# Performance work log

Measured on AMD Instinct MI355X. Metric: run time of the kernel, lower is better.

The kernel has to match this reference:

```python
import jax, jax.numpy as jnp
import numpy as np

N_NODES = 50000
N_EDGES = 800000
N_GRAPHS = 512
IN_FEATS = 256
HIDDEN = 128
OUT_FEATS = 128


def _lin(key, fan_in, fan_out):
    return jax.random.normal(key, (fan_in, fan_out), jnp.float32) * (1.0 / np.sqrt(fan_in))


def setup_inputs() -> dict:
    key = jax.random.key(0)
    ks = jax.random.split(key, 16)
    x = jax.random.normal(ks[0], (N_NODES, IN_FEATS), jnp.float32)
    edge_index = jax.random.randint(ks[1], (2, N_EDGES), 0, N_NODES, jnp.int32)
    batch = jnp.sort(jax.random.randint(ks[2], (N_NODES,), 0, N_GRAPHS, jnp.int32))
    return {
        "x": x,
        "edge_index": edge_index,
        "batch": batch,
        "num_graphs": N_GRAPHS,
        # TD branch GCN params
        "td_W1": _lin(ks[3], IN_FEATS, HIDDEN), "td_b1": jnp.zeros((HIDDEN,), jnp.float32),
        "td_W2": _lin(ks[4], HIDDEN, OUT_FEATS), "td_b2": jnp.zeros((OUT_FEATS,), jnp.float32),
        # BU branch GCN params
        "bu_W1": _lin(ks[5], IN_FEATS, HIDDEN), "bu_b1": jnp.zeros((HIDDEN,), jnp.float32),
        "bu_W2": _lin(ks[6], HIDDEN, OUT_FEATS), "bu_b2": jnp.zeros((OUT_FEATS,), jnp.float32),
        # proj_head: Linear(256,256) -> ReLU -> Linear(256,128)
        "pw1": _lin(ks[7], OUT_FEATS * 2, 256), "pb1": jnp.zeros((256,), jnp.float32),
        "pw2": _lin(ks[8], 256, 128), "pb2": jnp.zeros((128,), jnp.float32),
    }


def gcn_conv(h_in, W, b, src, dst, n_nodes):
    """PyG GCNConv: self-loops + symmetric normalization D^-1/2 (A+I) D^-1/2 X W + b."""
    h = h_in @ W  # [N, out]
    ones = jnp.ones(src.shape[0], h.dtype)
    deg = jax.ops.segment_sum(ones, dst, num_segments=n_nodes) + 1.0  # +1 for self-loop
    dinv = jax.lax.rsqrt(deg)  # deg >= 1 always
    norm = dinv[src] * dinv[dst]  # [E]
    agg = jax.ops.segment_sum(h[src] * norm[:, None], dst, num_segments=n_nodes)
    agg = agg + h * (dinv * dinv)[:, None]  # self-loop edge contribution
    return agg + b


def reference(x, edge_index, batch, num_graphs,
              td_W1, td_b1, td_W2, td_b2,
              bu_W1, bu_b1, bu_W2, bu_b2,
              pw1, pb1, pw2, pb2):
    n = x.shape[0]
    src, dst = edge_index[0], edge_index[1]

    def branch(W1, b1, W2, b2, s, d):
        h = jax.nn.relu(gcn_conv(x, W1, b1, s, d, n))
        # dropout is identity in eval mode
        h = gcn_conv(h, W2, b2, s, d, n)
        return jax.ops.segment_sum(h, batch, num_segments=num_graphs)  # global_add_pool

    td = branch(td_W1, td_b1, td_W2, td_b2, src, dst)
    bu = branch(bu_W1, bu_b1, bu_W2, bu_b2, dst, src)  # flipped edge_index
    h = jnp.concatenate([bu, td], axis=1)  # [G, 2*out_feats]
    h = jax.nn.relu(h @ pw1 + pb1) @ pw2 + pb2
    return h
```

## Files before the change

kernel.cpp:

```cpp
#include <hip/hip_runtime.h>

#define N_NODES 50000
#define N_PAD   50048
#define N_EDGES 800000
#define N_GRAPHS 512
#define F_IN 256
#define F_H 128
#define F_CAT 256

#define BSHIFT 9
#define NB 98
#define CAP 10240
#define EPB 3125

#define NPAIR 16
#define SLICE_C 16
#define POOL_STRIDE ((size_t)N_PAD * SLICE_C)
#define AGG_CHUNK 128
#define N_GROUPS (N_NODES / 4)

typedef __attribute__((ext_vector_type(8))) short short8;
typedef __attribute__((ext_vector_type(4))) float f32x4;
typedef unsigned int uint;
typedef unsigned short ushort;

static __device__ __forceinline__ ushort f2bf(float f) {
    uint u = __float_as_uint(f);
    u += 0x7FFF + ((u >> 16) & 1);
    return (ushort)(u >> 16);
}
static __device__ __forceinline__ float bflo(uint v) { return __uint_as_float(v << 16); }
static __device__ __forceinline__ float bfhi(uint v) { return __uint_as_float(v & 0xFFFF0000u); }
static __device__ __forceinline__ float bfu(ushort v) { return __uint_as_float((uint)v << 16); }

#define GLL(g, l) __builtin_amdgcn_global_load_lds( \
    (const __attribute__((address_space(1))) unsigned int*)(g), \
    (__attribute__((address_space(3))) unsigned int*)(l), 16, 0, 0)

__global__ __launch_bounds__(256) void csr_scatter_kernel(
        const int* __restrict__ ei, int* __restrict__ gcur,
        uint* __restrict__ ebuf_td, uint* __restrict__ ebuf_bu) {
    __shared__ int lcnt[256];
    __shared__ int lbase[256];
    int tid = threadIdx.x;
    lcnt[tid] = 0;
    __syncthreads();
    int e0 = blockIdx.x * EPB;
    for (int k = tid; k < EPB; k += 256) {
        int i = e0 + k;
        int s = ei[i], d = ei[N_EDGES + i];
        atomicAdd(&lcnt[d >> BSHIFT], 1);
        atomicAdd(&lcnt[128 + (s >> BSHIFT)], 1);
    }
    __syncthreads();
    if (tid < 2 * NB) {
        int dir = tid / NB, b = tid % NB;
        int c = lcnt[dir * 128 + b];
        lbase[dir * 128 + b] = c ? atomicAdd(&gcur[dir * NB + b], c) : 0;
    }
    __syncthreads();
    lcnt[tid] = 0;
    __syncthreads();
    for (int k = tid; k < EPB; k += 256) {
        int i = e0 + k;
        int s = ei[i], d = ei[N_EDGES + i];
        int bd = d >> BSHIFT, bs = s >> BSHIFT;
        int p = atomicAdd(&lcnt[bd], 1) + lbase[bd];
        ebuf_td[(size_t)bd * CAP + p] = (uint)s | ((uint)(d & 511) << 16);
        int q = atomicAdd(&lcnt[128 + bs], 1) + lbase[128 + bs];
        ebuf_bu[(size_t)bs * CAP + q] = (uint)d | ((uint)(s & 511) << 16);
    }
}

__global__ __launch_bounds__(256) void csr_build_kernel(
        const uint* __restrict__ ebuf_td, const uint* __restrict__ ebuf_bu,
        const int* __restrict__ gcur,
        int* off_td, int* off_bu, ushort* deg_td, ushort* deg_bu,
        float* dinv_td, float* dinv_bu, ushort* csr_td, ushort* csr_bu) {
    int b = blockIdx.x, dir = blockIdx.y;
    const uint* ebuf = dir ? ebuf_bu : ebuf_td;
    int* off     = dir ? off_bu : off_td;
    ushort* deg  = dir ? deg_bu : deg_td;
    float* dinv  = dir ? dinv_bu : dinv_td;
    ushort* csr  = dir ? csr_bu : csr_td;
    __shared__ int cntL[512], offL[512], sm[256];
    int tid = threadIdx.x;
    cntL[tid] = 0; cntL[tid + 256] = 0;
    __syncthreads();
    int rbeg = b * CAP;
    int rend = rbeg + gcur[dir * NB + b];
    for (int k = rbeg + tid; k < rend; k += 256)
        atomicAdd(&cntL[ebuf[k] >> 16], 1);
    __syncthreads();
    int a0 = cntL[tid * 2], a1 = cntL[tid * 2 + 1];
    int ps = a0 + a1;
    sm[tid] = ps;
    __syncthreads();
    for (int o = 1; o < 256; o <<= 1) {
        int u = (tid >= o) ? sm[tid - o] : 0;
        __syncthreads();
        sm[tid] += u;
        __syncthreads();
    }
    int excl = sm[tid] - ps;
    offL[tid * 2] = excl;
    offL[tid * 2 + 1] = excl + a0;
    __syncthreads();
    int nbase = b << BSHIFT;
#pragma unroll
    for (int j = 0; j < 2; j++) {
        int nloc = tid + j * 256;
        int n = nbase + nloc;
        if (n < N_NODES) {
            off[n] = rbeg + offL[nloc];
            int c = cntL[nloc];
            deg[n] = (ushort)c;
            dinv[n] = rsqrtf((float)c + 1.0f);
        }
    }
    if (b == NB - 1) {
        int n = N_NODES + tid;
        if (n < N_PAD) dinv[n] = 1.0f;
    }
    cntL[tid] = offL[tid];
    cntL[tid + 256] = offL[tid + 256];
    __syncthreads();
    for (int k = rbeg + tid; k < rend; k += 256) {
        uint e = ebuf[k];
        int slot = atomicAdd(&cntL[e >> 16], 1);
        csr[rbeg + slot] = (ushort)(e & 0xFFFF);
    }
}

__global__ void prep_w_kernel(const float* __restrict__ td_W1, const float* __restrict__ bu_W1,
                              const float* __restrict__ td_W2, const float* __restrict__ bu_W2,
                              ushort* __restrict__ Bt1, ushort* __restrict__ Wt2) {
    int n = blockIdx.x;
    int k = threadIdx.x;
    float w1 = (n < F_H) ? td_W1[(size_t)k * F_H + n] : bu_W1[(size_t)k * F_H + (n - F_H)];
    Bt1[(size_t)n * 256 + k] = f2bf(w1);
    if (k < 128) {
        float w2 = (n < F_H) ? bu_W2[(size_t)k * F_H + n]
                             : td_W2[(size_t)k * F_H + (n - F_H)];
        Wt2[(size_t)k * 256 + n] = f2bf(w2);
    }
}

__global__ __launch_bounds__(256) void gemm_mfma(
        const float* __restrict__ x, const ushort* __restrict__ Bt,
        ushort* __restrict__ C,
        const float* __restrict__ dinv_td, const float* __restrict__ dinv_bu) {
    __shared__ __align__(16) ushort As[128 * 32];
    __shared__ __align__(16) ushort Bs[128 * 32];
    int tid = threadIdx.x;
    int wave = tid >> 6, lane = tid & 63, quad = lane >> 4, l16 = lane & 15;
    size_t bm = (size_t)blockIdx.x * 128;
    size_t bn = (size_t)blockIdx.y * 128;
    int br = blockIdx.y;
    const float* dsel = br ? dinv_bu : dinv_td;

    f32x4 acc[2][8];
    const f32x4 z4 = {0.f, 0.f, 0.f, 0.f};
#pragma unroll
    for (int i = 0; i < 2; i++)
#pragma unroll
        for (int j = 0; j < 8; j++) acc[i][j] = z4;

    int ar = tid >> 3;
    int akq = (tid & 7) * 4;
    int cb0 = wave * 64;
    int cb1 = 256 + wave * 64;
    int c0 = cb0 + lane, c1 = cb1 + lane;
    int r0 = c0 >> 2, s0 = (c0 & 3) * 8;
    int r1 = c1 >> 2, s1 = (c1 & 3) * 8;
    const ushort* b0p = Bt + (bn + r0) * 256 + s0;
    const ushort* b1p = Bt + (bn + r1) * 256 + s1;
    ushort* lB0 = Bs + cb0 * 8;
    ushort* lB1 = Bs + cb1 * 8;

    for (int kb = 0; kb < 8; kb++) {
        int k0 = kb * 32;
        float4 av[4];
#pragma unroll
        for (int j = 0; j < 4; j++) {
            size_t grow = bm + ar + j * 32;
            if (grow < N_NODES)
                av[j] = *(const float4*)(x + grow * F_IN + k0 + akq);
            else
                av[j] = make_float4(0.f, 0.f, 0.f, 0.f);
        }
        __syncthreads();
        GLL(b0p + k0, lB0);
        GLL(b1p + k0, lB1);
#pragma unroll
        for (int j = 0; j < 4; j++) {
            ushort4 u;
            u.x = f2bf(av[j].x); u.y = f2bf(av[j].y);
            u.z = f2bf(av[j].z); u.w = f2bf(av[j].w);
            *(ushort4*)(As + (ar + j * 32) * 32 + akq) = u;
        }
        __syncthreads();
        short8 af0 = *(const short8*)(As + (wave * 32 + l16) * 32 + quad * 8);
        short8 af1 = *(const short8*)(As + (wave * 32 + 16 + l16) * 32 + quad * 8);
#pragma unroll
        for (int ct = 0; ct < 8; ct++) {
            short8 bfr = *(const short8*)(Bs + (ct * 16 + l16) * 32 + quad * 8);
            acc[0][ct] = __builtin_amdgcn_mfma_f32_16x16x32_bf16(af0, bfr, acc[0][ct], 0, 0, 0);
            acc[1][ct] = __builtin_amdgcn_mfma_f32_16x16x32_bf16(af1, bfr, acc[1][ct], 0, 0, 0);
        }
    }
#pragma unroll
    for (int rt = 0; rt < 2; rt++) {
#pragma unroll
        for (int r = 0; r < 4; r++) {
            size_t row = bm + wave * 32 + rt * 16 + quad * 4 + r;
            float dv = dsel[row];
#pragma unroll
            for (int ct = 0; ct < 8; ct++) {
                C[(size_t)(br * 8 + ct) * POOL_STRIDE + row * 16 + l16] =
                    f2bf(acc[rt][ct][r] * dv);
            }
        }
    }
}

static __device__ __forceinline__ void acc8(float a[8], uint4 v) {
    a[0] += bflo(v.x); a[1] += bfhi(v.x);
    a[2] += bflo(v.y); a[3] += bfhi(v.y);
    a[4] += bflo(v.z); a[5] += bfhi(v.z);
    a[6] += bflo(v.w); a[7] += bfhi(v.w);
}

__global__ __launch_bounds__(256, 8) void agg1s_kernel(
        const ushort* __restrict__ linS2, ushort* __restrict__ h1s2,
        const ushort* __restrict__ csr_td, const int* __restrict__ off_td,
        const ushort* __restrict__ deg_td, const float* __restrict__ dinv_td,
        const ushort* __restrict__ csr_bu, const int* __restrict__ off_bu,
        const ushort* __restrict__ deg_bu, const float* __restrict__ dinv_bu,
        const float* __restrict__ b_td, const float* __restrict__ b_bu) {
    int b = blockIdx.x;
    int pair = b & 15;
    int chunk = b >> 4;
    int br = pair >> 3, s = pair & 7;
    const ushort* csr = br ? csr_bu : csr_td;
    const int* off    = br ? off_bu : off_td;
    const ushort* deg = br ? deg_bu : deg_td;
    const float* dinv = br ? dinv_bu : dinv_td;
    const float* bias = br ? b_bu : b_td;
    const ushort* pool = linS2 + (size_t)pair * POOL_STRIDE;
    ushort* opool      = h1s2 + (size_t)pair * POOL_STRIDE;

    int tid = threadIdx.x;
    int lane = tid & 63, w = tid >> 6;
    int half = lane & 1, es = (lane >> 1) & 7, nj = lane >> 4;
    int wq = chunk * 4 + w;
    const int WPP = AGG_CHUNK * 4;
    int beg = (int)(((long long)wq * N_GROUPS) / WPP);
    int end = (int)(((long long)(wq + 1) * N_GROUPS) / WPP);
    float bs[8];
#pragma unroll
    for (int j = 0; j < 8; j++) bs[j] = bias[s * 16 + half * 8 + j];

    for (int gi = beg; gi < end; ++gi) {
        int n = gi * 4 + nj;
        int kb = off[n], ke = kb + deg[n];
        float a[8] = {0.f, 0.f, 0.f, 0.f, 0.f, 0.f, 0.f, 0.f};
        for (int k = kb + es; k < ke; k += 8) {
            int e = csr[k];
            uint4 v = *(const uint4*)(pool + (size_t)e * 16 + half * 8);
            acc8(a, v);
        }
#pragma unroll
        for (int st = 2; st <= 8; st <<= 1)
#pragma unroll
            for (int u = 0; u < 8; u++) a[u] += __shfl_xor(a[u], st);
        if (es == 0) {
            uint4 vs = *(const uint4*)(pool + (size_t)n * 16 + half * 8);
            acc8(a, vs);
            float dn = dinv[n];
            float o[8];
#pragma unroll
            for (int u = 0; u < 8; u++) o[u] = fmaxf(a[u] * dn + bs[u], 0.f) * dn;
            uint4 pk;
            pk.x = (uint)f2bf(o[0]) | ((uint)f2bf(o[1]) << 16);
            pk.y = (uint)f2bf(o[2]) | ((uint)f2bf(o[3]) << 16);
            pk.z = (uint)f2bf(o[4]) | ((uint)f2bf(o[5]) << 16);
            pk.w = (uint)f2bf(o[6]) | ((uint)f2bf(o[7]) << 16);
            *(uint4*)(opool + (size_t)n * 16 + half * 8) = pk;
        }
    }
}

__global__ __launch_bounds__(256, 8) void agg2s_kernel(
        const ushort* __restrict__ h1s2, float* __restrict__ pooled_pre,
        const int* __restrict__ batch,
        const ushort* __restrict__ csr_td, const int* __restrict__ off_td,
        const ushort* __restrict__ deg_td, const float* __restrict__ dinv_td,
        const ushort* __restrict__ csr_bu, const int* __restrict__ off_bu,
        const ushort* __restrict__ deg_bu, const float* __restrict__ dinv_bu) {
    int b = blockIdx.x;
    int pair = b & 15;
    int chunk = b >> 4;
    int br = pair >> 3, s = pair & 7;
    const ushort* csr = br ? csr_bu : csr_td;
    const int* off    = br ? off_bu : off_td;
    const ushort* deg = br ? deg_bu : deg_td;
    const float* dinv = br ? dinv_bu : dinv_td;
    const ushort* pool = h1s2 + (size_t)pair * POOL_STRIDE;

    int tid = threadIdx.x;
    int lane = tid & 63, w = tid >> 6;
    int half = lane & 1, es = (lane >> 1) & 7, nj = lane >> 4;
    int wq = chunk * 4 + w;
    const int WPP = AGG_CHUNK * 4;
    int beg = (int)(((long long)wq * N_GROUPS) / WPP);
    int end = (int)(((long long)(wq + 1) * N_GROUPS) / WPP);

    float acc[8] = {0.f, 0.f, 0.f, 0.f, 0.f, 0.f, 0.f, 0.f};
    int gcur = -1;
    int colbase = br * F_H + s * 16 + half * 8;

    for (int gi = beg; gi < end; ++gi) {
        int n = gi * 4 + nj;
        int kb = off[n], ke = kb + deg[n];
        float a[8] = {0.f, 0.f, 0.f, 0.f, 0.f, 0.f, 0.f, 0.f};
        for (int k = kb + es; k < ke; k += 8) {
            int e = csr[k];
            uint4 v = *(const uint4*)(pool + (size_t)e * 16 + half * 8);
            acc8(a, v);
        }
#pragma unroll
        for (int st = 2; st <= 8; st <<= 1)
#pragma unroll
            for (int u = 0; u < 8; u++) a[u] += __shfl_xor(a[u], st);
        if (es == 0) {
            uint4 vs = *(const uint4*)(pool + (size_t)n * 16 + half * 8);
            acc8(a, vs);
            float dn = dinv[n];
            int g = batch[n];
            if (g != gcur) {
                if (gcur >= 0) {
                    float* pp = &pooled_pre[(size_t)gcur * F_CAT + colbase];
#pragma unroll
                    for (int u = 0; u < 8; u++) unsafeAtomicAdd(pp + u, acc[u]);
                }
                gcur = g;
#pragma unroll
                for (int u = 0; u < 8; u++) acc[u] = 0.f;
            }
#pragma unroll
            for (int u = 0; u < 8; u++) acc[u] += a[u] * dn;
        }
    }
    if (es == 0 && gcur >= 0) {
        float* pp = &pooled_pre[(size_t)gcur * F_CAT + colbase];
#pragma unroll
        for (int u = 0; u < 8; u++) unsafeAtomicAdd(pp + u, acc[u]);
    }
}

__global__ __launch_bounds__(256) void head_kernel(
        const float* __restrict__ pooled_pre, const int* __restrict__ batch,
        const ushort* __restrict__ Wt2,
        const float* __restrict__ td_b2, const float* __restrict__ bu_b2,
        const float* __restrict__ pw1, const float* __restrict__ pb1,
        const float* __restrict__ pw2, const float* __restrict__ pb2,
        float* __restrict__ out) {
    int g = blockIdx.x;
    int tid = threadIdx.x;
    __shared__ float row[256], z[256], hid[256];
    row[tid] = pooled_pre[(size_t)g * 256 + tid];
    int lo = 0, hi = N_NODES;
    while (lo < hi) { int m = (lo + hi) >> 1; if (batch[m] < g) lo = m + 1; else hi = m; }
    int start = lo;
    lo = start; hi = N_NODES;
    while (lo < hi) { int m = (lo + hi) >> 1; if (batch[m] < g + 1) lo = m + 1; else hi = m; }
    float cnt = (float)(lo - start);
    __syncthreads();
    const float* rsel = (tid < 128) ? (row + F_H) : row;
    float b2 = (tid < 128) ? bu_b2[tid] : td_b2[tid - F_H];
    float acc = cnt * b2;
    for (int k = 0; k < F_H; k++) acc += rsel[k] * bfu(Wt2[(size_t)k * 256 + tid]);
    z[tid] = acc;
    __syncthreads();
    float h = pb1[tid];
    for (int k = 0; k < 256; k++) h += z[k] * pw1[(size_t)k * 256 + tid];
    hid[tid] = fmaxf(h, 0.f);
    __syncthreads();
    if (tid < 128) {
        float o = pb2[tid];
        for (int k = 0; k < 256; k++) o += hid[k] * pw2[(size_t)k * 128 + tid];
        out[(size_t)g * 128 + tid] = o;
    }
}

extern "C" void kernel_launch(void* const* d_in, const int* in_sizes, int n_in,
                              void* d_out, int out_size, void* d_ws, size_t ws_size,
                              hipStream_t stream) {
    const float* x     = (const float*)d_in[0];
    const int*   ei    = (const int*)d_in[1];
    const int*   batch = (const int*)d_in[2];
    const float* td_W1 = (const float*)d_in[4];
    const float* td_b1 = (const float*)d_in[5];
    const float* td_W2 = (const float*)d_in[6];
    const float* td_b2 = (const float*)d_in[7];
    const float* bu_W1 = (const float*)d_in[8];
    const float* bu_b1 = (const float*)d_in[9];
    const float* bu_W2 = (const float*)d_in[10];
    const float* bu_b2 = (const float*)d_in[11];
    const float* pw1   = (const float*)d_in[12];
    const float* pb1   = (const float*)d_in[13];
    const float* pw2   = (const float*)d_in[14];
    const float* pb2   = (const float*)d_in[15];
    float* out = (float*)d_out;

    char* p = (char*)d_ws;
    auto alloc = [&](size_t bytes) { void* r = (void*)p; p += (bytes + 255) & ~(size_t)255; return r; };
    char* zreg = (char*)alloc(1024 + (size_t)N_GRAPHS * F_CAT * sizeof(float));
    int* gcur = (int*)zreg;
    float* pooled_pre = (float*)(zreg + 1024);
    uint* ebuf_td = (uint*)alloc((size_t)NB * CAP * sizeof(uint));
    uint* ebuf_bu = (uint*)alloc((size_t)NB * CAP * sizeof(uint));
    ushort* csr_td = (ushort*)alloc((size_t)NB * CAP * sizeof(ushort));
    ushort* csr_bu = (ushort*)alloc((size_t)NB * CAP * sizeof(ushort));
    int* off_td = (int*)alloc((size_t)N_NODES * sizeof(int));
    int* off_bu = (int*)alloc((size_t)N_NODES * sizeof(int));
    ushort* deg_td = (ushort*)alloc((size_t)N_NODES * sizeof(ushort));
    ushort* deg_bu = (ushort*)alloc((size_t)N_NODES * sizeof(ushort));
    float* dinv_td = (float*)alloc((size_t)N_PAD * sizeof(float));
    float* dinv_bu = (float*)alloc((size_t)N_PAD * sizeof(float));
    ushort* Bt1 = (ushort*)alloc((size_t)256 * 256 * sizeof(ushort));
    ushort* Wt2 = (ushort*)alloc((size_t)128 * 256 * sizeof(ushort));
    ushort* linb = (ushort*)alloc((size_t)NPAIR * POOL_STRIDE * sizeof(ushort));
    ushort* h1s  = (ushort*)alloc((size_t)NPAIR * POOL_STRIDE * sizeof(ushort));

    hipMemsetAsync(zreg, 0, 1024 + (size_t)N_GRAPHS * F_CAT * sizeof(float), stream);

    prep_w_kernel<<<256, 256, 0, stream>>>(td_W1, bu_W1, td_W2, bu_W2, Bt1, Wt2);

    csr_scatter_kernel<<<N_EDGES / EPB, 256, 0, stream>>>(ei, gcur, ebuf_td, ebuf_bu);
    csr_build_kernel<<<dim3(NB, 2), 256, 0, stream>>>(ebuf_td, ebuf_bu, gcur,
        off_td, off_bu, deg_td, deg_bu, dinv_td, dinv_bu, csr_td, csr_bu);

    dim3 gg(N_PAD / 128, 2);
    gemm_mfma<<<gg, 256, 0, stream>>>(x, Bt1, linb, dinv_td, dinv_bu);
    agg1s_kernel<<<NPAIR * AGG_CHUNK, 256, 0, stream>>>(linb, h1s,
        csr_td, off_td, deg_td, dinv_td, csr_bu, off_bu, deg_bu, dinv_bu, td_b1, bu_b1);

    agg2s_kernel<<<NPAIR * AGG_CHUNK, 256, 0, stream>>>(h1s, pooled_pre, batch,
        csr_td, off_td, deg_td, dinv_td, csr_bu, off_bu, deg_bu, dinv_bu);

    head_kernel<<<N_GRAPHS, 256, 0, stream>>>(pooled_pre, batch, Wt2,
        td_b2, bu_b2, pw1, pb1, pw2, pb2, out);
}
```

Measured before the change: 405.6 us.

## Split neighbor gathers by source-node half to localize feature-table working set

```diff
diff --git a/kernel.cpp b/kernel.cpp
--- a/kernel.cpp
+++ b/kernel.cpp
@@ -13,14 +13,12 @@
 #define CAP 10240
 #define EPB 3125
 
-#define NPAIR 16
-#define SLICE_C 16
-#define POOL_STRIDE ((size_t)N_PAD * SLICE_C)
-#define AGG_CHUNK 128
-#define N_GROUPS (N_NODES / 4)
+#define HALF 25024
+#define POOL64 ((size_t)N_PAD * 64)
 
 typedef __attribute__((ext_vector_type(8))) short short8;
 typedef __attribute__((ext_vector_type(4))) float f32x4;
+typedef __attribute__((ext_vector_type(4))) unsigned int u32x4;
 typedef unsigned int uint;
 typedef unsigned short ushort;
 
@@ -76,24 +74,29 @@
         const uint* __restrict__ ebuf_td, const uint* __restrict__ ebuf_bu,
         const int* __restrict__ gcur,
         int* off_td, int* off_bu, ushort* deg_td, ushort* deg_bu,
+        ushort* dlo_td, ushort* dlo_bu,
         float* dinv_td, float* dinv_bu, ushort* csr_td, ushort* csr_bu) {
     int b = blockIdx.x, dir = blockIdx.y;
     const uint* ebuf = dir ? ebuf_bu : ebuf_td;
     int* off     = dir ? off_bu : off_td;
     ushort* deg  = dir ? deg_bu : deg_td;
+    ushort* dlo  = dir ? dlo_bu : dlo_td;
     float* dinv  = dir ? dinv_bu : dinv_td;
     ushort* csr  = dir ? csr_bu : csr_td;
-    __shared__ int cntL[512], offL[512], sm[256];
-    int tid = threadIdx.x;
-    cntL[tid] = 0; cntL[tid + 256] = 0;
+    __shared__ int cntL[1024], offL[1024], sm[256];
+    int tid = threadIdx.x;
+    for (int i = tid; i < 1024; i += 256) cntL[i] = 0;
     __syncthreads();
     int rbeg = b * CAP;
     int rend = rbeg + gcur[dir * NB + b];
-    for (int k = rbeg + tid; k < rend; k += 256)
-        atomicAdd(&cntL[ebuf[k] >> 16], 1);
-    __syncthreads();
-    int a0 = cntL[tid * 2], a1 = cntL[tid * 2 + 1];
-    int ps = a0 + a1;
+    for (int k = rbeg + tid; k < rend; k += 256) {
+        uint e = ebuf[k];
+        atomicAdd(&cntL[((e >> 16) << 1) | ((e & 0xFFFFu) >= HALF)], 1);
+    }
+    __syncthreads();
+    int a0 = cntL[tid * 4], a1 = cntL[tid * 4 + 1];
+    int a2 = cntL[tid * 4 + 2], a3 = cntL[tid * 4 + 3];
+    int ps = a0 + a1 + a2 + a3;
     sm[tid] = ps;
     __syncthreads();
     for (int o = 1; o < 256; o <<= 1) {
@@ -103,8 +106,10 @@
         __syncthreads();
     }
     int excl = sm[tid] - ps;
-    offL[tid * 2] = excl;
-    offL[tid * 2 + 1] = excl + a0;
+    offL[tid * 4]     = excl;
+    offL[tid * 4 + 1] = excl + a0;
+    offL[tid * 4 + 2] = excl + a0 + a1;
+    offL[tid * 4 + 3] = excl + a0 + a1 + a2;
     __syncthreads();
     int nbase = b << BSHIFT;
 #pragma unroll
@@ -112,23 +117,26 @@
         int nloc = tid + j * 256;
         int n = nbase + nloc;
         if (n < N_NODES) {
-            off[n] = rbeg + offL[nloc];
-            int c = cntL[nloc];
-            deg[n] = (ushort)c;
-            dinv[n] = rsqrtf((float)c + 1.0f);
+            off[n] = rbeg + offL[nloc * 2];
+            int cl = cntL[nloc * 2], ch = cntL[nloc * 2 + 1];
+            deg[n] = (ushort)(cl + ch);
+            dlo[n] = (ushort)cl;
+            dinv[n] = rsqrtf((float)(cl + ch) + 1.0f);
         }
     }
     if (b == NB - 1) {
         int n = N_NODES + tid;
         if (n < N_PAD) dinv[n] = 1.0f;
     }
-    cntL[tid] = offL[tid];
-    cntL[tid + 256] = offL[tid + 256];
+    __syncthreads();
+    for (int i = tid; i < 1024; i += 256) cntL[i] = offL[i];
     __syncthreads();
     for (int k = rbeg + tid; k < rend; k += 256) {
         uint e = ebuf[k];
-        int slot = atomicAdd(&cntL[e >> 16], 1);
-        csr[rbeg + slot] = (ushort)(e & 0xFFFF);
+        uint src = e & 0xFFFFu;
+        int key = (int)(((e >> 16) << 1) | (src >= HALF));
+        int slot = atomicAdd(&cntL[key], 1);
+        csr[rbeg + slot] = (ushort)src;
     }
 }
 
@@ -217,8 +225,9 @@
             float dv = dsel[row];
 #pragma unroll
             for (int ct = 0; ct < 8; ct++) {
-                C[(size_t)(br * 8 + ct) * POOL_STRIDE + row * 16 + l16] =
-                    f2bf(acc[rt][ct][r] * dv);
+                size_t addr = (size_t)((br << 1) | (ct >> 2)) * POOL64
+                            + row * 64 + (ct & 3) * 16 + l16;
+                C[addr] = f2bf(acc[rt][ct][r] * dv);
             }
         }
     }
@@ -231,118 +240,181 @@
     a[6] += bflo(v.w); a[7] += bfhi(v.w);
 }
 
-__global__ __launch_bounds__(256, 8) void agg1s_kernel(
-        const ushort* __restrict__ linS2, ushort* __restrict__ h1s2,
+static __device__ __forceinline__ void gather64(
+        const ushort* __restrict__ pool, const ushort* __restrict__ csr,
+        int kb, int ke, int es, int lc, float a[8]) {
+    for (int k = kb + es; k < ke; k += 8) {
+        int e = (int)__builtin_nontemporal_load(csr + k);
+        uint4 v = *(const uint4*)(pool + (size_t)e * 64 + lc * 8);
+        acc8(a, v);
+    }
+}
+
+__global__ __launch_bounds__(256, 8) void agg1a_kernel(
+        const ushort* __restrict__ linb, float* __restrict__ partial,
         const ushort* __restrict__ csr_td, const int* __restrict__ off_td,
-        const ushort* __restrict__ deg_td, const float* __restrict__ dinv_td,
+        const ushort* __restrict__ dlo_td,
         const ushort* __restrict__ csr_bu, const int* __restrict__ off_bu,
-        const ushort* __restrict__ deg_bu, const float* __restrict__ dinv_bu,
-        const float* __restrict__ b_td, const float* __restrict__ b_bu) {
-    int b = blockIdx.x;
-    int pair = b & 15;
-    int chunk = b >> 4;
-    int br = pair >> 3, s = pair & 7;
+        const ushort* __restrict__ dlo_bu) {
+    int blk = blockIdx.x;
+    int combo = blk & 3;
+    int br = combo >> 1;
     const ushort* csr = br ? csr_bu : csr_td;
     const int* off    = br ? off_bu : off_td;
+    const ushort* dlo = br ? dlo_bu : dlo_td;
+    const ushort* pool = linb + (size_t)combo * POOL64;
+    float* pp = partial + (size_t)combo * POOL64;
+
+    int tid = threadIdx.x;
+    int lane = tid & 63, w = tid >> 6;
+    int es = lane >> 3, lc = lane & 7;
+    int wq = (blk >> 2) * 4 + w;
+    int beg = (int)(((long long)wq * N_NODES) / 2048);
+    int end = (int)(((long long)(wq + 1) * N_NODES) / 2048);
+
+    for (int n = beg; n < end; ++n) {
+        int kb = __builtin_nontemporal_load(off + n);
+        int kl = (int)__builtin_nontemporal_load(dlo + n);
+        float a[8] = {0.f, 0.f, 0.f, 0.f, 0.f, 0.f, 0.f, 0.f};
+        gather64(pool, csr, kb, kb + kl, es, lc, a);
+#pragma unroll
+        for (int st = 8; st <= 32; st <<= 1)
+#pragma unroll
+            for (int u = 0; u < 8; u++) a[u] += __shfl_xor(a[u], st);
+        if (es == 0) {
+            if (n < HALF) {
+                uint4 v = *(const uint4*)(pool + (size_t)n * 64 + lc * 8);
+                acc8(a, v);
+            }
+            f32x4 q0 = {a[0], a[1], a[2], a[3]};
+            f32x4 q1 = {a[4], a[5], a[6], a[7]};
+            f32x4* dst = (f32x4*)(pp + (size_t)n * 64 + lc * 8);
+            __builtin_nontemporal_store(q0, dst);
+            __builtin_nontemporal_store(q1, dst + 1);
+        }
+    }
+}
+
+__global__ __launch_bounds__(256, 8) void agg1b_kernel(
+        const ushort* __restrict__ linb, const float* __restrict__ partial,
+        ushort* __restrict__ h1s,
+        const ushort* __restrict__ csr_td, const int* __restrict__ off_td,
+        const ushort* __restrict__ dlo_td, const ushort* __restrict__ deg_td,
+        const ushort* __restrict__ csr_bu, const int* __restrict__ off_bu,
+        const ushort* __restrict__ dlo_bu, const ushort* __restrict__ deg_bu,
+        const float* __restrict__ dinv_td, const float* __restrict__ dinv_bu,
+        const float* __restrict__ b_td, const float* __restrict__ b_bu) {
+    int blk = blockIdx.x;
+    int combo = blk & 3;
+    int br = combo >> 1, s = combo & 1;
+    const ushort* csr = br ? csr_bu : csr_td;
+    const int* off    = br ? off_bu : off_td;
+    const ushort* dlo = br ? dlo_bu : dlo_td;
     const ushort* deg = br ? deg_bu : deg_td;
     const float* dinv = br ? dinv_bu : dinv_td;
     const float* bias = br ? b_bu : b_td;
-    const ushort* pool = linS2 + (size_t)pair * POOL_STRIDE;
-    ushort* opool      = h1s2 + (size_t)pair * POOL_STRIDE;
+    const ushort* pool = linb + (size_t)combo * POOL64;
+    const float* pp = partial + (size_t)combo * POOL64;
+    ushort* op = h1s + (size_t)combo * POOL64;
 
     int tid = threadIdx.x;
     int lane = tid & 63, w = tid >> 6;
-    int half = lane & 1, es = (lane >> 1) & 7, nj = lane >> 4;
-    int wq = chunk * 4 + w;
-    const int WPP = AGG_CHUNK * 4;
-    int beg = (int)(((long long)wq * N_GROUPS) / WPP);
-    int end = (int)(((long long)(wq + 1) * N_GROUPS) / WPP);
+    int es = lane >> 3, lc = lane & 7;
+    int wq = (blk >> 2) * 4 + w;
+    int beg = (int)(((long long)wq * N_NODES) / 2048);
+    int end = (int)(((long long)(wq + 1) * N_NODES) / 2048);
     float bs[8];
 #pragma unroll
-    for (int j = 0; j < 8; j++) bs[j] = bias[s * 16 + half * 8 + j];
-
-    for (int gi = beg; gi < end; ++gi) {
-        int n = gi * 4 + nj;
-        int kb = off[n], ke = kb + deg[n];
+    for (int u = 0; u < 8; u++) bs[u] = bias[s * 64 + lc * 8 + u];
+
+    for (int n = beg; n < end; ++n) {
+        int kb = __builtin_nontemporal_load(off + n);
+        int kl = (int)__builtin_nontemporal_load(dlo + n);
+        int kd = (int)__builtin_nontemporal_load(deg + n);
         float a[8] = {0.f, 0.f, 0.f, 0.f, 0.f, 0.f, 0.f, 0.f};
-        for (int k = kb + es; k < ke; k += 8) {
-            int e = csr[k];
-            uint4 v = *(const uint4*)(pool + (size_t)e * 16 + half * 8);
-            acc8(a, v);
-        }
-#pragma unroll
-        for (int st = 2; st <= 8; st <<= 1)
+        gather64(pool, csr, kb + kl, kb + kd, es, lc, a);
+#pragma unroll
+        for (int st = 8; st <= 32; st <<= 1)
 #pragma unroll
             for (int u = 0; u < 8; u++) a[u] += __shfl_xor(a[u], st);
         if (es == 0) {
-            uint4 vs = *(const uint4*)(pool + (size_t)n * 16 + half * 8);
-            acc8(a, vs);
-            float dn = dinv[n];
+            if (n >= HALF) {
+                uint4 v = *(const uint4*)(pool + (size_t)n * 64 + lc * 8);
+                acc8(a, v);
+            }
+            const f32x4* sp = (const f32x4*)(pp + (size_t)n * 64 + lc * 8);
+            f32x4 q0 = __builtin_nontemporal_load(sp);
+            f32x4 q1 = __builtin_nontemporal_load(sp + 1);
+            a[0] += q0.x; a[1] += q0.y; a[2] += q0.z; a[3] += q0.w;
+            a[4] += q1.x; a[5] += q1.y; a[6] += q1.z; a[7] += q1.w;
+            float dn = __builtin_nontemporal_load(dinv + n);
             float o[8];
 #pragma unroll
             for (int u = 0; u < 8; u++) o[u] = fmaxf(a[u] * dn + bs[u], 0.f) * dn;
-            uint4 pk;
+            u32x4 pk;
             pk.x = (uint)f2bf(o[0]) | ((uint)f2bf(o[1]) << 16);
             pk.y = (uint)f2bf(o[2]) | ((uint)f2bf(o[3]) << 16);
             pk.z = (uint)f2bf(o[4]) | ((uint)f2bf(o[5]) << 16);
             pk.w = (uint)f2bf(o[6]) | ((uint)f2bf(o[7]) << 16);
-            *(uint4*)(opool + (size_t)n * 16 + half * 8) = pk;
-        }
-    }
-}
-
-__global__ __launch_bounds__(256, 8) void agg2s_kernel(
-        const ushort* __restrict__ h1s2, float* __restrict__ pooled_pre,
+            __builtin_nontemporal_store(pk, (u32x4*)(op + (size_t)n * 64 + lc * 8));
+        }
+    }
+}
+
+__global__ __launch_bounds__(256, 8) void agg2h_kernel(
+        const ushort* __restrict__ h1s, float* __restrict__ pooled_pre,
         const int* __restrict__ batch,
         const ushort* __restrict__ csr_td, const int* __restrict__ off_td,
-        const ushort* __restrict__ deg_td, const float* __restrict__ dinv_td,
+        const ushort* __restrict__ dlo_td, const ushort* __restrict__ deg_td,
         const ushort* __restrict__ csr_bu, const int* __restrict__ off_bu,
-        const ushort* __restrict__ deg_bu, const float* __restrict__ dinv_bu) {
-    int b = blockIdx.x;
-    int pair = b & 15;
-    int chunk = b >> 4;
-    int br = pair >> 3, s = pair & 7;
+        const ushort* __restrict__ dlo_bu, const ushort* __restrict__ deg_bu,
+        const float* __restrict__ dinv_td, const float* __restrict__ dinv_bu) {
+    int blk = blockIdx.x;
+    int combo = blk & 7;
+    int br = combo >> 2, s = (combo >> 1) & 1, h = combo & 1;
     const ushort* csr = br ? csr_bu : csr_td;
     const int* off    = br ? off_bu : off_td;
+    const ushort* dlo = br ? dlo_bu : dlo_td;
     const ushort* deg = br ? deg_bu : deg_td;
     const float* dinv = br ? dinv_bu : dinv_td;
-    const ushort* pool = h1s2 + (size_t)pair * POOL_STRIDE;
+    const ushort* pool = h1s + (size_t)((br << 1) | s) * POOL64;
 
     int tid = threadIdx.x;
     int lane = tid & 63, w = tid >> 6;
-    int half = lane & 1, es = (lane >> 1) & 7, nj = lane >> 4;
-    int wq = chunk * 4 + w;
-    const int WPP = AGG_CHUNK * 4;
-    int beg = (int)(((long long)wq * N_GROUPS) / WPP);
-    int end = (int)(((long long)(wq + 1) * N_GROUPS) / WPP);
+    int es = lane >> 3, lc = lane & 7;
+    int wq = (blk >> 3) * 4 + w;
+    int beg = (int)(((long long)wq * N_NODES) / 1024);
+    int end = (int)(((long long)(wq + 1) * N_NODES) / 1024);
+    int colbase = br * F_H + s * 64 + lc * 8;
 
     float acc[8] = {0.f, 0.f, 0.f, 0.f, 0.f, 0.f, 0.f, 0.f};
     int gcur = -1;
-    int colbase = br * F_H + s * 16 + half * 8;
-
-    for (int gi = beg; gi < end; ++gi) {
-        int n = gi * 4 + nj;
-        int kb = off[n], ke = kb + deg[n];
+
+    for (int n = beg; n < end; ++n) {
+        int kb = __builtin_nontemporal_load(off + n);
+        int kl = (int)__builtin_nontemporal_load(dlo + n);
+        int kd = (int)__builtin_nontemporal_load(deg + n);
+        int k0 = h ? kb + kl : kb;
+        int k1 = h ? kb + kd : kb + kl;
         float a[8] = {0.f, 0.f, 0.f, 0.f, 0.f, 0.f, 0.f, 0.f};
-        for (int k = kb + es; k < ke; k += 8) {
-            int e = csr[k];
-            uint4 v = *(const uint4*)(pool + (size_t)e * 16 + half * 8);
-            acc8(a, v);
-        }
-#pragma unroll
-        for (int st = 2; st <= 8; st <<= 1)
+        gather64(pool, csr, k0, k1, es, lc, a);
+#pragma unroll
+        for (int st = 8; st <= 32; st <<= 1)
 #pragma unroll
             for (int u = 0; u < 8; u++) a[u] += __shfl_xor(a[u], st);
         if (es == 0) {
-            uint4 vs = *(const uint4*)(pool + (size_t)n * 16 + half * 8);
-            acc8(a, vs);
-            float dn = dinv[n];
-            int g = batch[n];
+            bool selfmine = h ? (n >= HALF) : (n < HALF);
+            if (selfmine) {
+                uint4 v = *(const uint4*)(pool + (size_t)n * 64 + lc * 8);
+                acc8(a, v);
+            }
+            float dn = __builtin_nontemporal_load(dinv + n);
+            int g = __builtin_nontemporal_load(batch + n);
             if (g != gcur) {
                 if (gcur >= 0) {
-                    float* pp = &pooled_pre[(size_t)gcur * F_CAT + colbase];
-#pragma unroll
-                    for (int u = 0; u < 8; u++) unsafeAtomicAdd(pp + u, acc[u]);
+                    float* q = &pooled_pre[(size_t)gcur * F_CAT + colbase];
+#pragma unroll
+                    for (int u = 0; u < 8; u++) unsafeAtomicAdd(q + u, acc[u]);
                 }
                 gcur = g;
 #pragma unroll
@@ -352,10 +424,10 @@
             for (int u = 0; u < 8; u++) acc[u] += a[u] * dn;
         }
     }
-    if (es == 0 && gcur >= 0) {
-        float* pp = &pooled_pre[(size_t)gcur * F_CAT + colbase];
-#pragma unroll
-        for (int u = 0; u < 8; u++) unsafeAtomicAdd(pp + u, acc[u]);
+    if ((lane >> 3) == 0 && gcur >= 0) {
+        float* q = &pooled_pre[(size_t)gcur * F_CAT + colbase];
+#pragma unroll
+        for (int u = 0; u < 8; u++) unsafeAtomicAdd(q + u, acc[u]);
     }
 }
 
@@ -419,20 +491,23 @@
     char* zreg = (char*)alloc(1024 + (size_t)N_GRAPHS * F_CAT * sizeof(float));
     int* gcur = (int*)zreg;
     float* pooled_pre = (float*)(zreg + 1024);
-    uint* ebuf_td = (uint*)alloc((size_t)NB * CAP * sizeof(uint));
-    uint* ebuf_bu = (uint*)alloc((size_t)NB * CAP * sizeof(uint));
+    float* partial = (float*)alloc((size_t)4 * POOL64 * sizeof(float));
+    uint* ebuf_td = (uint*)partial;
+    uint* ebuf_bu = ebuf_td + (size_t)NB * CAP;
     ushort* csr_td = (ushort*)alloc((size_t)NB * CAP * sizeof(ushort));
     ushort* csr_bu = (ushort*)alloc((size_t)NB * CAP * sizeof(ushort));
     int* off_td = (int*)alloc((size_t)N_NODES * sizeof(int));
     int* off_bu = (int*)alloc((size_t)N_NODES * sizeof(int));
     ushort* deg_td = (ushort*)alloc((size_t)N_NODES * sizeof(ushort));
     ushort* deg_bu = (ushort*)alloc((size_t)N_NODES * sizeof(ushort));
+    ushort* dlo_td = (ushort*)alloc((size_t)N_NODES * sizeof(ushort));
+    ushort* dlo_bu = (ushort*)alloc((size_t)N_NODES * sizeof(ushort));
     float* dinv_td = (float*)alloc((size_t)N_PAD * sizeof(float));
     float* dinv_bu = (float*)alloc((size_t)N_PAD * sizeof(float));
     ushort* Bt1 = (ushort*)alloc((size_t)256 * 256 * sizeof(ushort));
     ushort* Wt2 = (ushort*)alloc((size_t)128 * 256 * sizeof(ushort));
-    ushort* linb = (ushort*)alloc((size_t)NPAIR * POOL_STRIDE * sizeof(ushort));
-    ushort* h1s  = (ushort*)alloc((size_t)NPAIR * POOL_STRIDE * sizeof(ushort));
+    ushort* linb = (ushort*)alloc((size_t)4 * POOL64 * sizeof(ushort));
+    ushort* h1s  = (ushort*)alloc((size_t)4 * POOL64 * sizeof(ushort));
 
     hipMemsetAsync(zreg, 0, 1024 + (size_t)N_GRAPHS * F_CAT * sizeof(float), stream);
 
@@ -440,15 +515,21 @@
 
     csr_scatter_kernel<<<N_EDGES / EPB, 256, 0, stream>>>(ei, gcur, ebuf_td, ebuf_bu);
     csr_build_kernel<<<dim3(NB, 2), 256, 0, stream>>>(ebuf_td, ebuf_bu, gcur,
-        off_td, off_bu, deg_td, deg_bu, dinv_td, dinv_bu, csr_td, csr_bu);
+        off_td, off_bu, deg_td, deg_bu, dlo_td, dlo_bu,
+        dinv_td, dinv_bu, csr_td, csr_bu);
 
     dim3 gg(N_PAD / 128, 2);
     gemm_mfma<<<gg, 256, 0, stream>>>(x, Bt1, linb, dinv_td, dinv_bu);
-    agg1s_kernel<<<NPAIR * AGG_CHUNK, 256, 0, stream>>>(linb, h1s,
-        csr_td, off_td, deg_td, dinv_td, csr_bu, off_bu, deg_bu, dinv_bu, td_b1, bu_b1);
-
-    agg2s_kernel<<<NPAIR * AGG_CHUNK, 256, 0, stream>>>(h1s, pooled_pre, batch,
-        csr_td, off_td, deg_td, dinv_td, csr_bu, off_bu, deg_bu, dinv_bu);
+
+    agg1a_kernel<<<2048, 256, 0, stream>>>(linb, partial,
+        csr_td, off_td, dlo_td, csr_bu, off_bu, dlo_bu);
+    agg1b_kernel<<<2048, 256, 0, stream>>>(linb, partial, h1s,
+        csr_td, off_td, dlo_td, deg_td, csr_bu, off_bu, dlo_bu, deg_bu,
+        dinv_td, dinv_bu, td_b1, bu_b1);
+
+    agg2h_kernel<<<2048, 256, 0, stream>>>(h1s, pooled_pre, batch,
+        csr_td, off_td, dlo_td, deg_td, csr_bu, off_bu, dlo_bu, deg_bu,
+        dinv_td, dinv_bu);
 
     head_kernel<<<N_GRAPHS, 256, 0, stream>>>(pooled_pre, batch, Wt2,
         td_b2, bu_b2, pw1, pb1, pw2, pb2, out);
```

New measurement: 544.4 us. 1.34x slower.
